# Optimization experiments

Measured on AMD Instinct MI355X. Metric: run time of the kernel, lower is better.

The kernel has to match this reference:

```python
import jax, jax.numpy as jnp
import numpy as np


def setup_inputs() -> dict:
    key = jax.random.key(0)
    kx, kq, kk, kv = jax.random.split(key, 4)
    B, S, F, D = 4, 4096, 512, 64
    x = jax.random.normal(kx, (B, S, F), dtype=jnp.float32)
    Wq = jax.random.normal(kq, (F, D), dtype=jnp.float32) * 0.05
    Wk = jax.random.normal(kk, (F, D), dtype=jnp.float32) * 0.05
    Wv = jax.random.normal(kv, (F, D), dtype=jnp.float32) * 0.05
    return {"x": x, "Wq": Wq, "Wk": Wk, "Wv": Wv}


def reference(x, Wq, Wk, Wv):
    # x: [B,S,F]; Wq/Wk/Wv: [F,D]
    q = jnp.einsum('bsf,fd->bsd', x, Wq)
    k = jnp.einsum('bsf,fd->bsd', x, Wk)
    v = jnp.einsum('bsf,fd->bsd', x, Wv)
    scale = 1.0 / jnp.sqrt(jnp.asarray(Wq.shape[-1], dtype=x.dtype))
    scores = jnp.einsum('bqd,bkd->bqk', q, k) * scale  # [B,S,S]
    weights = jax.nn.softmax(scores, axis=-1)
    return jnp.einsum('bqk,bkd->bqd', weights, v)
```

## Files before the change

### kernel.cpp

```cpp
#include <hip/hip_runtime.h>

constexpr int Bc = 4, Sc = 4096, Fc = 512, Dc = 64;
constexpr int SPLIT = 8;
constexpr int KT = 64;
constexpr int TILES = (Sc / SPLIT) / KT;

typedef __attribute__((ext_vector_type(8)))  short  short8;
typedef __attribute__((ext_vector_type(4)))  float  float4v;
typedef __attribute__((ext_vector_type(16))) float  float16v;

__device__ inline unsigned short f2bf(float f) {
    union { float f; unsigned u; } v; v.f = f;
    unsigned r = v.u + 0x7FFF + ((v.u >> 16) & 1);
    return (unsigned short)(r >> 16);
}
__device__ inline unsigned pk2(float a, float b) {
    union { float f; unsigned u; } x, y; x.f = a; y.f = b;
    unsigned ra = x.u + 0x7FFF + ((x.u >> 16) & 1);
    unsigned rb = y.u + 0x7FFF + ((y.u >> 16) & 1);
    return (ra >> 16) | (rb & 0xFFFF0000u);
}
__device__ inline float exp2fast(float x) {
#if defined(__has_builtin) && __has_builtin(__builtin_amdgcn_exp2f)
    return __builtin_amdgcn_exp2f(x);
#else
    return __expf(x * 0.69314718055994531f);
#endif
}

__global__ __launch_bounds__(256) void prep_kernel(
    const float* __restrict__ Wq, const float* __restrict__ Wk,
    const float* __restrict__ Wv, unsigned short* __restrict__ Wf)
{
    int wi = blockIdx.x * 256 + threadIdx.x;
    int lane = wi & 63;
    int kc = (wi >> 6) & 15;
    int nt = wi >> 10;
    int lm = lane & 15, quad = lane >> 4;
    int n = nt * 16 + lm;
    const float* W = (n < 64) ? Wq : (n < 128) ? Wk : Wv;
    int nc = n & 63;
    float scale = (n < 64) ? 0.18033688011112042f : 1.0f;
    int kbase = kc * 32 + quad * 8;
    union { uint4 v; unsigned short s[8]; } tmp;
    #pragma unroll
    for (int j = 0; j < 8; ++j)
        tmp.s[j] = f2bf(W[(size_t)(kbase + j) * Dc + nc] * scale);
    *(uint4*)&Wf[(size_t)wi * 8] = tmp.v;
}

__global__ __launch_bounds__(256) void qkv_kernel(
    const float* __restrict__ x, const unsigned short* __restrict__ Wf,
    unsigned short* __restrict__ Qb, unsigned short* __restrict__ Kb,
    unsigned short* __restrict__ Vtb)
{
    __shared__ __align__(16) unsigned short Xs[2][16][72];
    __shared__ __align__(16) unsigned short Ot[16][200];
    const int t = threadIdx.x;
    const int lane = t & 63, w = t >> 6;
    const int lm = lane & 15, quad = lane >> 4;
    const int row0 = blockIdx.x * 16;
    const int sr = t >> 4, sc4 = (t & 15) * 4;

    float4 xv;
    auto load_x = [&](int k0) {
        xv = *(const float4*)&x[(size_t)(row0 + sr) * Fc + k0 + sc4];
    };
    load_x(0);

    float4v acc[3];
    #pragma unroll
    for (int n = 0; n < 3; ++n) acc[n] = float4v{0.f, 0.f, 0.f, 0.f};

    int buf = 0;
    #pragma unroll
    for (int k0 = 0; k0 < Fc; k0 += 64, buf ^= 1) {
        uint2 pk;
        pk.x = pk2(xv.x, xv.y); pk.y = pk2(xv.z, xv.w);
        *(uint2*)&Xs[buf][sr][sc4] = pk;
        __syncthreads();
        if (k0 + 64 < Fc) load_x(k0 + 64);

        short8 af[2];
        #pragma unroll
        for (int h = 0; h < 2; ++h)
            af[h] = *(const short8*)&Xs[buf][lm][h * 32 + quad * 8];

        #pragma unroll
        for (int n = 0; n < 3; ++n) {
            const int nt = 3 * w + n;
            #pragma unroll
            for (int h = 0; h < 2; ++h) {
                const int kchunk = (k0 >> 5) + h;
                short8 bf_ = *(const short8*)&Wf[(size_t)((nt * 16 + kchunk) * 64 + lane) * 8];
                acc[n] = __builtin_amdgcn_mfma_f32_16x16x32_bf16(af[h], bf_, acc[n], 0, 0, 0);
            }
        }
    }

    __syncthreads();
    #pragma unroll
    for (int n = 0; n < 3; ++n)
        #pragma unroll
        for (int r = 0; r < 4; ++r)
            Ot[quad * 4 + r][(3 * w + n) * 16 + lm] = f2bf(acc[n][r]);
    __syncthreads();

    {
        const int r2 = t >> 4, c2 = (t & 15) * 4;
        *(uint2*)&Qb[(size_t)(row0 + r2) * Dc + c2] = *(const uint2*)&Ot[r2][c2];
        *(uint2*)&Kb[(size_t)(row0 + r2) * Dc + c2] = *(const uint2*)&Ot[r2][64 + c2];
    }
    {
        const int d = t >> 2, s4 = (t & 3) * 4;
        union { uint2 v; unsigned short s[4]; } tmp;
        #pragma unroll
        for (int j = 0; j < 4; ++j) tmp.s[j] = Ot[s4 + j][128 + d];
        const int bb = row0 >> 12, s0r = row0 & (Sc - 1);
        *(uint2*)&Vtb[((size_t)bb * Dc + d) * Sc + s0r + s4] = tmp.v;
    }
}

__global__ __launch_bounds__(256) void attn_kernel(
    const unsigned short* __restrict__ Qb, const unsigned short* __restrict__ Kb,
    const unsigned short* __restrict__ Vtb,
    float* __restrict__ Op, float* __restrict__ lp)
{
    constexpr int PD = 72;
    __shared__ __align__(16) char smem[36864];
    unsigned short* Kt = (unsigned short*)smem;
    unsigned short* Vt = (unsigned short*)(smem + 9216);
    unsigned short* Pt = (unsigned short*)(smem + 18432);

    const int t = threadIdx.x;
    const int lane = t & 63, w = t >> 6;
    const int l31 = lane & 31, lh = lane >> 5;
    const int b = blockIdx.y, z = blockIdx.z;
    const int q0 = blockIdx.x * 128 + w * 32;
    const size_t qkbase = (size_t)b * Sc * Dc;
    const size_t vbase  = (size_t)b * Dc * Sc;
    const int k0base = z * (Sc / SPLIT);

    short8 qf[4];
    #pragma unroll
    for (int c = 0; c < 4; ++c)
        qf[c] = *(const short8*)&Qb[qkbase + (size_t)(q0 + l31) * Dc + c * 16 + lh * 8];

    float16v O0, O1;
    #pragma unroll
    for (int r = 0; r < 16; ++r) { O0[r] = 0.f; O1[r] = 0.f; }
    float l_i = 0.f;

    const int skey = t >> 2, sd = (t & 3) * 16;
    uint4 kr[2], vr[2];
    auto load_tile = [&](int k0) {
        const unsigned short* kp = Kb + qkbase + (size_t)(k0 + skey) * Dc + sd;
        const unsigned short* vp = Vtb + vbase + (size_t)skey * Sc + k0 + sd;
        kr[0] = *(const uint4*)kp;  kr[1] = *(const uint4*)(kp + 8);
        vr[0] = *(const uint4*)vp;  vr[1] = *(const uint4*)(vp + 8);
    };
    load_tile(k0base);

    for (int kt = 0; kt < TILES; ++kt) {
        __syncthreads();
        *(uint4*)&Kt[skey * PD + sd]     = kr[0];
        *(uint4*)&Kt[skey * PD + sd + 8] = kr[1];
        *(uint4*)&Vt[skey * PD + sd]     = vr[0];
        *(uint4*)&Vt[skey * PD + sd + 8] = vr[1];
        __syncthreads();
        if (kt + 1 < TILES) load_tile(k0base + (kt + 1) * KT);

        float16v s0, s1;
        #pragma unroll
        for (int r = 0; r < 16; ++r) { s0[r] = 0.f; s1[r] = 0.f; }
        #pragma unroll
        for (int c = 0; c < 4; ++c) {
            short8 a0 = *(const short8*)&Kt[(l31) * PD + c * 16 + lh * 8];
            short8 a1 = *(const short8*)&Kt[(32 + l31) * PD + c * 16 + lh * 8];
            s0 = __builtin_amdgcn_mfma_f32_32x32x16_bf16(a0, qf[c], s0, 0, 0, 0);
            s1 = __builtin_amdgcn_mfma_f32_32x32x16_bf16(a1, qf[c], s1, 0, 0, 0);
        }

        #pragma unroll
        for (int r = 0; r < 16; ++r) {
            float p0 = exp2fast(s0[r]); s0[r] = p0; l_i += p0;
            float p1 = exp2fast(s1[r]); s1[r] = p1; l_i += p1;
        }

        unsigned short* prow = &Pt[w * 32 * PD + l31 * PD];
        #pragma unroll
        for (int g = 0; g < 4; ++g) {
            uint2 v;
            v.x = pk2(s0[4 * g], s0[4 * g + 1]); v.y = pk2(s0[4 * g + 2], s0[4 * g + 3]);
            *(uint2*)&prow[8 * g + 4 * lh] = v;
            v.x = pk2(s1[4 * g], s1[4 * g + 1]); v.y = pk2(s1[4 * g + 2], s1[4 * g + 3]);
            *(uint2*)&prow[32 + 8 * g + 4 * lh] = v;
        }

        #pragma unroll
        for (int c = 0; c < 4; ++c) {
            short8 pb  = *(const short8*)&prow[c * 16 + lh * 8];
            short8 va0 = *(const short8*)&Vt[(l31) * PD + c * 16 + lh * 8];
            short8 va1 = *(const short8*)&Vt[(32 + l31) * PD + c * 16 + lh * 8];
            O0 = __builtin_amdgcn_mfma_f32_32x32x16_bf16(va0, pb, O0, 0, 0, 0);
            O1 = __builtin_amdgcn_mfma_f32_32x32x16_bf16(va1, pb, O1, 0, 0, 0);
        }
    }

    l_i += __shfl_xor(l_i, 32);

    __syncthreads();
    float* Of = (float*)(smem + w * 8704);
    #pragma unroll
    for (int r = 0; r < 16; ++r) {
        int d0 = (r & 3) + 8 * (r >> 2) + 4 * lh;
        Of[l31 * 68 + d0]      = O0[r];
        Of[l31 * 68 + 32 + d0] = O1[r];
    }
    const size_t obase = ((size_t)(z * Bc + b) * Sc + q0) * Dc;
    const int qr = lane >> 4, c4 = (lane & 15) * 4;
    #pragma unroll
    for (int i = 0; i < 8; ++i) {
        int q = i * 4 + qr;
        *(float4*)&Op[obase + (size_t)q * Dc + c4] = *(const float4*)&Of[q * 68 + c4];
    }
    if (lane < 32)
        lp[(z * Bc + b) * Sc + q0 + l31] = l_i;
}

__global__ __launch_bounds__(256) void combine_kernel(
    const float* __restrict__ Op, const float* __restrict__ lp,
    float* __restrict__ out)
{
    const int BS = Bc * Sc;
    int tid = blockIdx.x * 256 + threadIdx.x;
    int bq = tid >> 4, dc = (tid & 15) * 4;
    float L = 0.f;
    #pragma unroll
    for (int zz = 0; zz < SPLIT; ++zz) L += lp[zz * BS + bq];
    float inv = 1.f / L;
    size_t o = (size_t)bq * Dc + dc;
    size_t stride = (size_t)BS * Dc;
    float4 r = {0.f, 0.f, 0.f, 0.f};
    #pragma unroll
    for (int zz = 0; zz < SPLIT; ++zz) {
        float4 pz = *(const float4*)&Op[o + zz * stride];
        r.x += pz.x; r.y += pz.y; r.z += pz.z; r.w += pz.w;
    }
    r.x *= inv; r.y *= inv; r.z *= inv; r.w *= inv;
    *(float4*)&out[o] = r;
}

extern "C" void kernel_launch(void* const* d_in, const int* in_sizes, int n_in,
                              void* d_out, int out_size, void* d_ws, size_t ws_size,
                              hipStream_t stream) {
    const float* x  = (const float*)d_in[0];
    const float* Wq = (const float*)d_in[1];
    const float* Wk = (const float*)d_in[2];
    const float* Wv = (const float*)d_in[3];
    float* out = (float*)d_out;

    char* p = (char*)d_ws;
    unsigned short* Wf  = (unsigned short*)p;  p += (size_t)192 * Fc * 2;
    unsigned short* Qb  = (unsigned short*)p;  p += (size_t)Bc * Sc * Dc * 2;
    unsigned short* Kb  = (unsigned short*)p;  p += (size_t)Bc * Sc * Dc * 2;
    unsigned short* Vtb = (unsigned short*)p;  p += (size_t)Bc * Sc * Dc * 2;
    float* lp = (float*)p;                     p += (size_t)SPLIT * Bc * Sc * 4;
    float* Op = (float*)p;

    prep_kernel<<<48, 256, 0, stream>>>(Wq, Wk, Wv, Wf);
    qkv_kernel<<<Bc * Sc / 16, 256, 0, stream>>>(x, Wf, Qb, Kb, Vtb);
    attn_kernel<<<dim3(Sc / 128, Bc, SPLIT), 256, 0, stream>>>(Qb, Kb, Vtb, Op, lp);
    combine_kernel<<<(Bc * Sc * 16) / 256, 256, 0, stream>>>(Op, lp, out);
}
```

Baseline: 145.3 us.

## Double-buffer K/V via direct global-to-LDS loads and keep P in registers

Replaces the register-staged K/V tile copy with global_load_lds direct DMA into a double-buffered, XOR-swizzled LDS layout, so the next tile's loads overlap compute and need only one barrier per iteration. The softmax probabilities are converted to the MFMA B operand in registers with permlane32 swaps instead of a round trip through LDS. s_setprio hints are also added around the MFMA blocks. In exchange it uses more LDS per block and depends on the swizzle and permlane mapping being right, and the global_load_lds completion ordering with the single barrier may be fragile.

```diff
diff --git a/kernel.cpp b/kernel.cpp
--- a/kernel.cpp
+++ b/kernel.cpp
@@ -8,6 +8,7 @@
 typedef __attribute__((ext_vector_type(8)))  short  short8;
 typedef __attribute__((ext_vector_type(4)))  float  float4v;
 typedef __attribute__((ext_vector_type(16))) float  float16v;
+typedef __attribute__((ext_vector_type(2)))  unsigned int uint2v;
 
 __device__ inline unsigned short f2bf(float f) {
     union { float f; unsigned u; } v; v.f = f;
@@ -25,6 +26,20 @@
     return __builtin_amdgcn_exp2f(x);
 #else
     return __expf(x * 0.69314718055994531f);
+#endif
+}
+
+__device__ inline void swap32(unsigned& a, unsigned& b) {
+#if defined(__has_builtin) && __has_builtin(__builtin_amdgcn_permlane32_swap)
+    uint2v r = __builtin_amdgcn_permlane32_swap(a, b, false, false);
+    a = r[0]; b = r[1];
+#else
+    unsigned ax = (unsigned)__shfl_xor((int)a, 32);
+    unsigned bx = (unsigned)__shfl_xor((int)b, 32);
+    int upper = (threadIdx.x & 32) != 0;
+    unsigned na = upper ? bx : a;
+    unsigned nb = upper ? b  : ax;
+    a = na; b = nb;
 #endif
 }
 
@@ -126,11 +141,7 @@
     const unsigned short* __restrict__ Vtb,
     float* __restrict__ Op, float* __restrict__ lp)
 {
-    constexpr int PD = 72;
-    __shared__ __align__(16) char smem[36864];
-    unsigned short* Kt = (unsigned short*)smem;
-    unsigned short* Vt = (unsigned short*)(smem + 9216);
-    unsigned short* Pt = (unsigned short*)(smem + 18432);
+    __shared__ __align__(16) char smem[34816];
 
     const int t = threadIdx.x;
     const int lane = t & 63, w = t >> 6;
@@ -151,35 +162,64 @@
     for (int r = 0; r < 16; ++r) { O0[r] = 0.f; O1[r] = 0.f; }
     float l_i = 0.f;
 
-    const int skey = t >> 2, sd = (t & 3) * 16;
-    uint4 kr[2], vr[2];
-    auto load_tile = [&](int k0) {
-        const unsigned short* kp = Kb + qkbase + (size_t)(k0 + skey) * Dc + sd;
-        const unsigned short* vp = Vtb + vbase + (size_t)skey * Sc + k0 + sd;
-        kr[0] = *(const uint4*)kp;  kr[1] = *(const uint4*)(kp + 8);
-        vr[0] = *(const uint4*)vp;  vr[1] = *(const uint4*)(vp + 8);
+    const int rowInW = lane >> 3;
+    const int srcChunk = (lane & 7) ^ rowInW;
+    auto stage = [&](int p, int k0) {
+        char* base = smem + p * 16384;
+        #pragma unroll
+        for (int j = 0; j < 2; ++j) {
+            const int row = w * 16 + j * 8 + rowInW;
+            const unsigned short* gk = Kb + qkbase + (size_t)(k0 + row) * Dc + srcChunk * 8;
+            const unsigned short* gv = Vtb + vbase + (size_t)row * Sc + k0 + srcChunk * 8;
+            __builtin_amdgcn_global_load_lds(
+                (const __attribute__((address_space(1))) void*)gk,
+                (__attribute__((address_space(3))) void*)(base + (w * 16 + j * 8) * 128),
+                16, 0, 0);
+            __builtin_amdgcn_global_load_lds(
+                (const __attribute__((address_space(1))) void*)gv,
+                (__attribute__((address_space(3))) void*)(base + 8192 + (w * 16 + j * 8) * 128),
+                16, 0, 0);
+        }
     };
-    load_tile(k0base);
-
-    for (int kt = 0; kt < TILES; ++kt) {
-        __syncthreads();
-        *(uint4*)&Kt[skey * PD + sd]     = kr[0];
-        *(uint4*)&Kt[skey * PD + sd + 8] = kr[1];
-        *(uint4*)&Vt[skey * PD + sd]     = vr[0];
-        *(uint4*)&Vt[skey * PD + sd + 8] = vr[1];
-        __syncthreads();
-        if (kt + 1 < TILES) load_tile(k0base + (kt + 1) * KT);
+
+    const int rx = l31 & 7;
+    auto rd = [&](const char* buf, int row, int cc) -> short8 {
+        return *(const short8*)(buf + row * 128 + (cc ^ rx) * 16);
+    };
+
+    auto mk_pb = [&](const float16v& s, int g) -> short8 {
+        unsigned X0 = pk2(s[8 * g + 0], s[8 * g + 1]);
+        unsigned X1 = pk2(s[8 * g + 2], s[8 * g + 3]);
+        unsigned Y0 = pk2(s[8 * g + 4], s[8 * g + 5]);
+        unsigned Y1 = pk2(s[8 * g + 6], s[8 * g + 7]);
+        swap32(X0, Y0);
+        swap32(X1, Y1);
+        union { unsigned u[4]; short8 s8; } r;
+        r.u[0] = X0; r.u[1] = X1; r.u[2] = Y0; r.u[3] = Y1;
+        return r.s8;
+    };
+
+    stage(0, k0base);
+    __syncthreads();
+
+    int p = 0;
+    for (int kt = 0; kt < TILES; ++kt, p ^= 1) {
+        if (kt + 1 < TILES) stage(p ^ 1, k0base + (kt + 1) * KT);
+        const char* kb = smem + p * 16384;
+        const char* vb = kb + 8192;
 
         float16v s0, s1;
         #pragma unroll
         for (int r = 0; r < 16; ++r) { s0[r] = 0.f; s1[r] = 0.f; }
+        __builtin_amdgcn_s_setprio(1);
         #pragma unroll
         for (int c = 0; c < 4; ++c) {
-            short8 a0 = *(const short8*)&Kt[(l31) * PD + c * 16 + lh * 8];
-            short8 a1 = *(const short8*)&Kt[(32 + l31) * PD + c * 16 + lh * 8];
+            short8 a0 = rd(kb, l31,      2 * c + lh);
+            short8 a1 = rd(kb, 32 + l31, 2 * c + lh);
             s0 = __builtin_amdgcn_mfma_f32_32x32x16_bf16(a0, qf[c], s0, 0, 0, 0);
             s1 = __builtin_amdgcn_mfma_f32_32x32x16_bf16(a1, qf[c], s1, 0, 0, 0);
         }
+        __builtin_amdgcn_s_setprio(0);
 
         #pragma unroll
         for (int r = 0; r < 16; ++r) {
@@ -187,29 +227,27 @@
             float p1 = exp2fast(s1[r]); s1[r] = p1; l_i += p1;
         }
 
-        unsigned short* prow = &Pt[w * 32 * PD + l31 * PD];
-        #pragma unroll
-        for (int g = 0; g < 4; ++g) {
-            uint2 v;
-            v.x = pk2(s0[4 * g], s0[4 * g + 1]); v.y = pk2(s0[4 * g + 2], s0[4 * g + 3]);
-            *(uint2*)&prow[8 * g + 4 * lh] = v;
-            v.x = pk2(s1[4 * g], s1[4 * g + 1]); v.y = pk2(s1[4 * g + 2], s1[4 * g + 3]);
-            *(uint2*)&prow[32 + 8 * g + 4 * lh] = v;
-        }
-
+        short8 pb0 = mk_pb(s0, 0);
+        short8 pb1 = mk_pb(s0, 1);
+        short8 pb2 = mk_pb(s1, 0);
+        short8 pb3 = mk_pb(s1, 1);
+
+        __builtin_amdgcn_s_setprio(1);
         #pragma unroll
         for (int c = 0; c < 4; ++c) {
-            short8 pb  = *(const short8*)&prow[c * 16 + lh * 8];
-            short8 va0 = *(const short8*)&Vt[(l31) * PD + c * 16 + lh * 8];
-            short8 va1 = *(const short8*)&Vt[(32 + l31) * PD + c * 16 + lh * 8];
+            short8 pb  = (c == 0) ? pb0 : (c == 1) ? pb1 : (c == 2) ? pb2 : pb3;
+            short8 va0 = rd(vb, l31,      2 * c + lh);
+            short8 va1 = rd(vb, 32 + l31, 2 * c + lh);
             O0 = __builtin_amdgcn_mfma_f32_32x32x16_bf16(va0, pb, O0, 0, 0, 0);
             O1 = __builtin_amdgcn_mfma_f32_32x32x16_bf16(va1, pb, O1, 0, 0, 0);
         }
+        __builtin_amdgcn_s_setprio(0);
+
+        __syncthreads();
     }
 
     l_i += __shfl_xor(l_i, 32);
 
-    __syncthreads();
     float* Of = (float*)(smem + w * 8704);
     #pragma unroll
     for (int r = 0; r < 16; ++r) {
```

Measured after the change: 121.6 us. 16.3% less time.
